# Kernel tuning notes

Measured on AMD Instinct MI355X. Metric: run time of the kernel, lower is better.

## Reference

```python
import jax, jax.numpy as jnp
import numpy as np

E = 1024   # n_embd
H = 16     # n_heads
D = 64     # head_dim
G = 4      # n_kv_groups
F = 4096   # ffn hidden_dim
V = 32000  # vocab
L = 4      # n_layers (all full_attention)
B = 1
T = 2048
ROT = 16   # partial_rotary_factor 0.25 * head_dim 64, rounded to even
EPS = 1e-6
THETA = 10000.0


def rope_tables(seq_len):
    # matches compute_rope_params: inv_freq over even indices of rotary_dim
    inv_freq = 1.0 / (THETA ** (jnp.arange(0, ROT, 2, dtype=jnp.float32) / ROT))
    ang = jnp.arange(seq_len, dtype=jnp.float32)[:, None] * inv_freq[None, :]
    ang = jnp.concatenate([ang, ang], axis=1)  # [T, ROT]
    return jnp.cos(ang), jnp.sin(ang)


def rmsnorm(x, w):
    # torch RMSNorm: x * rsqrt(mean(x^2)+eps) * (1 + weight)
    xf = x.astype(jnp.float32)
    n = xf * jax.lax.rsqrt(jnp.mean(xf * xf, axis=-1, keepdims=True) + EPS)
    return (n * (1.0 + w)).astype(x.dtype)


def apply_rope(x, cos, sin):
    # x: [B, h, T, D]; cos/sin: [1, 1, T, ROT]; partial rotary on first ROT dims
    x_rot, x_pass = x[..., :ROT], x[..., ROT:]
    x1, x2 = x_rot[..., :ROT // 2], x_rot[..., ROT // 2:]
    rotated = jnp.concatenate([-x2, x1], axis=-1)
    return jnp.concatenate([x_rot * cos + rotated * sin, x_pass], axis=-1)


def _forward(tokens, emb, Wq, Wk, Wv, Wo, qn, kn, n1, n2, f1, f2, f3, fn, head):
    cos, sin = rope_tables(T)
    cos = cos[None, None]  # [1,1,T,ROT]
    sin = sin[None, None]
    mask = jnp.triu(jnp.ones((T, T), dtype=bool), k=1)  # True = masked
    scale = D ** -0.5
    x = emb[tokens]  # [B,T,E]

    def block(x, p):
        wq, wk, wv, wo, qw, kw, w1, w2, g1, g2, g3 = p
        h = rmsnorm(x, w1)
        # fused Q + gate projection -> [B,T,H,2D], chunk on last dim
        qg = (h @ wq).reshape(B, T, H, 2 * D)
        q = qg[..., :D].transpose(0, 2, 1, 3)            # [B,H,T,D]
        gate = qg[..., D:].reshape(B, T, H * D)          # [B,T,H*D]
        k = (h @ wk).reshape(B, T, G, D).transpose(0, 2, 1, 3)  # [B,G,T,D]
        v = (h @ wv).reshape(B, T, G, D).transpose(0, 2, 1, 3)
        q = rmsnorm(q, qw)
        k = rmsnorm(k, kw)
        q = apply_rope(q, cos, sin)
        k = apply_rope(k, cos, sin)
        k = jnp.repeat(k, H // G, axis=1)  # GQA expand -> [B,H,T,D]
        v = jnp.repeat(v, H // G, axis=1)
        scores = jnp.einsum('bhqd,bhkd->bhqk', q, k)
        scores = jnp.where(mask, -jnp.inf, scores) * scale
        w = jax.nn.softmax(scores.astype(jnp.float32), axis=-1).astype(q.dtype)
        ctx = jnp.einsum('bhqk,bhkd->bhqd', w, v)
        ctx = ctx.transpose(0, 2, 1, 3).reshape(B, T, H * D)
        ctx = ctx * jax.nn.sigmoid(gate)
        x = x + ctx @ wo
        h2 = rmsnorm(x, w2)
        ff = (jax.nn.silu(h2 @ g1) * (h2 @ g2)) @ g3
        return x + ff, None

    params = (Wq, Wk, Wv, Wo, qn, kn, n1, n2, f1, f2, f3)
    x, _ = jax.lax.scan(block, x, params)
    return rmsnorm(x, fn) @ head  # logits [B,T,V]


def setup_inputs() -> dict:
    key = jax.random.key(0)
    ks = jax.random.split(key, 16)
    s = 0.02
    rn = lambda k, shape, sc=s: jax.random.normal(k, shape, jnp.float32) * sc
    return {
        'tokens': jax.random.randint(ks[0], (B, T), 0, V),
        'emb': rn(ks[1], (V, E)),
        'Wq': rn(ks[2], (L, E, 2 * H * D)),
        'Wk': rn(ks[3], (L, E, G * D)),
        'Wv': rn(ks[4], (L, E, G * D)),
        'Wo': rn(ks[5], (L, H * D, E)),
        'qn': rn(ks[6], (L, D)),
        'kn': rn(ks[7], (L, D)),
        'n1': rn(ks[8], (L, E)),
        'n2': rn(ks[9], (L, E)),
        'f1': rn(ks[10], (L, E, F)),
        'f2': rn(ks[11], (L, E, F)),
        'f3': rn(ks[12], (L, F, E)),
        'fn': rn(ks[13], (E,)),
        'head': rn(ks[14], (E, V)),
    }


def reference(tokens, emb, Wq, Wk, Wv, Wo, qn, kn, n1, n2, f1, f2, f3, fn, head):
    return _forward(tokens, emb, Wq, Wk, Wv, Wo, qn, kn, n1, n2, f1, f2, f3, fn, head)
```

## Files before the change

kernel.cpp:

```cpp
#include <hip/hip_runtime.h>

#define T_LEN 2048
#define E_DIM 1024
#define H_N 16
#define G_N 4
#define D_H 64
#define F_DIM 4096
#define V_SZ 32000
#define L_N 4

typedef __attribute__((ext_vector_type(8))) __bf16 bf16x8;
typedef __attribute__((ext_vector_type(4))) float f32x4;

__device__ __forceinline__ unsigned short f2bf(float f){
  unsigned int u = __float_as_uint(f);
  unsigned int r = (u + 0x7FFFu + ((u >> 16) & 1u)) >> 16;
  return (unsigned short)r;
}

__device__ __forceinline__ f32x4 mfma16(bf16x8 a, bf16x8 b, f32x4 c){
  return __builtin_amdgcn_mfma_f32_16x16x32_bf16(a, b, c, 0, 0, 0);
}

__device__ __forceinline__ void gl16(const void* g, void* l){
  __builtin_amdgcn_global_load_lds((const __attribute__((address_space(1))) void*)g,
                                   (__attribute__((address_space(3))) void*)l, 16, 0, 0);
}

#define SBAR() __builtin_amdgcn_s_barrier()
#define LGK0() do{ asm volatile("s_waitcnt lgkmcnt(0)" ::: "memory"); __builtin_amdgcn_sched_barrier(0); }while(0)
#define VMC4() do{ asm volatile("s_waitcnt vmcnt(4)" ::: "memory"); __builtin_amdgcn_sched_barrier(0); }while(0)
#define VMC0() do{ asm volatile("s_waitcnt vmcnt(0)" ::: "memory"); __builtin_amdgcn_sched_barrier(0); }while(0)

#define QSCALE 0.1803368801111183f

__global__ __launch_bounds__(256) void embed_k(const float* __restrict__ emb,
                                               const int* __restrict__ tokens,
                                               float* __restrict__ x){
  int t = blockIdx.x;
  int tok = tokens[t];
  const float4* src = (const float4*)(emb + (size_t)tok * E_DIM);
  float4* dst = (float4*)(x + (size_t)t * E_DIM);
  dst[threadIdx.x] = src[threadIdx.x];
}

__global__ __launch_bounds__(256) void transpose_bf16(const float* __restrict__ src,
                                                      unsigned short* __restrict__ dst,
                                                      int R, int C){
  __shared__ float tile[32][33];
  int c0 = blockIdx.x * 32, r0 = blockIdx.y * 32;
  int tx = threadIdx.x & 31, ty = threadIdx.x >> 5;
  for (int i = 0; i < 4; i++){
    int r = ty + i * 8;
    tile[r][tx] = src[(size_t)(r0 + r) * C + c0 + tx];
  }
  __syncthreads();
  for (int i = 0; i < 4; i++){
    int r = ty + i * 8;
    dst[(size_t)(c0 + r) * R + r0 + tx] = f2bf(tile[tx][r]);
  }
}

__device__ __forceinline__ void tr32(const float* __restrict__ src, unsigned short* __restrict__ dst,
                                     int R, int C, int bx, int by, float* tile ){
  int c0 = bx * 32, r0 = by * 32;
  int tx = threadIdx.x & 31, ty = threadIdx.x >> 5;
  for (int i = 0; i < 4; i++){
    int r = ty + i * 8;
    tile[r * 33 + tx] = src[(size_t)(r0 + r) * C + c0 + tx];
  }
  __syncthreads();
  for (int i = 0; i < 4; i++){
    int r = ty + i * 8;
    dst[(size_t)(c0 + r) * R + r0 + tx] = f2bf(tile[tx * 33 + r]);
  }
}

__global__ __launch_bounds__(256) void prep_weights(const float* __restrict__ Wq, const float* __restrict__ Wk,
                                                    const float* __restrict__ Wv, const float* __restrict__ Wo,
                                                    const float* __restrict__ f1, const float* __restrict__ f2,
                                                    const float* __restrict__ f3,
                                                    unsigned short* __restrict__ wt_qkv,
                                                    unsigned short* __restrict__ wt_o,
                                                    unsigned short* __restrict__ wt_f12i,
                                                    unsigned short* __restrict__ wt_f3){
  __shared__ float sh[1100];
  int id = blockIdx.x;
  if (id < 2048){ tr32(Wq, wt_qkv, 1024, 2048, id & 63, id >> 6, sh); return; }
  id -= 2048;
  if (id < 256){ tr32(Wk, wt_qkv + 2048 * 1024, 1024, 256, id & 7, id >> 3, sh); return; }
  id -= 256;
  if (id < 256){ tr32(Wv, wt_qkv + 2304 * 1024, 1024, 256, id & 7, id >> 3, sh); return; }
  id -= 256;
  if (id < 1024){ tr32(Wo, wt_o, 1024, 1024, id & 31, id >> 5, sh); return; }
  id -= 1024;
  if (id < 4096){ tr32(f3, wt_f3, 4096, 1024, id & 31, id >> 5, sh); return; }
  id -= 4096;
  {
    int q = id & 255, kb = id >> 8;
    float* t1 = sh; float* t2 = sh + 32 * 17;
    int c = threadIdx.x & 15, kk0 = threadIdx.x >> 4;
    for (int p = 0; p < 2; p++){
      int kk = p * 16 + kk0;
      t1[kk * 17 + c] = f1[(size_t)(kb * 32 + kk) * F_DIM + q * 16 + c];
      t2[kk * 17 + c] = f2[(size_t)(kb * 32 + kk) * F_DIM + q * 16 + c];
    }
    __syncthreads();
    int kk = threadIdx.x & 31, rb = threadIdx.x >> 5;
    for (int i = 0; i < 4; i++){
      int r = i * 8 + rb;
      float v = (r < 16) ? t1[kk * 17 + r] : t2[kk * 17 + (r - 16)];
      wt_f12i[(size_t)(q * 32 + r) * 1024 + kb * 32 + kk] = f2bf(v);
    }
  }
}

__global__ __launch_bounds__(256) void rmsnorm_k(const float* __restrict__ x,
                                                 const float* __restrict__ w,
                                                 unsigned short* __restrict__ out){
  const int t = blockIdx.x, tid = threadIdx.x;
  const float4 v = ((const float4*)(x + (size_t)t * E_DIM))[tid];
  float ss = v.x*v.x + v.y*v.y + v.z*v.z + v.w*v.w;
  for (int m = 1; m < 64; m <<= 1) ss += __shfl_xor(ss, m);
  __shared__ float red[4];
  if ((tid & 63) == 0) red[tid >> 6] = ss;
  __syncthreads();
  ss = red[0] + red[1] + red[2] + red[3];
  const float r = rsqrtf(ss * (1.0f / E_DIM) + 1e-6f);
  const float4 wv = ((const float4*)w)[tid];
  ushort4 o;
  o.x = f2bf(v.x * r * (1.0f + wv.x));
  o.y = f2bf(v.y * r * (1.0f + wv.y));
  o.z = f2bf(v.z * r * (1.0f + wv.z));
  o.w = f2bf(v.w * r * (1.0f + wv.w));
  ((ushort4*)(out + (size_t)t * E_DIM))[tid] = o;
}

template<bool ADD>
__global__ __launch_bounds__(256) void gemm64_bt(const unsigned short* __restrict__ A,
                                                 const unsigned short* __restrict__ Bt,
                                                 float* __restrict__ C,
                                                 int M, int N, int K){
  __shared__ unsigned short As[64 * 32];
  __shared__ unsigned short Bs[128 * 32];
  const int tid = threadIdx.x;
  const int lane = tid & 63, w = tid >> 6;
  const int l15 = lane & 15, l4 = lane >> 4;

  const int chunk = gridDim.x >> 3;
  const int wgid = (blockIdx.x & 7) * chunk + (blockIdx.x >> 3);
  const int nm = M >> 6;
  const int bm = wgid % nm, bn = wgid / nm;
  const int m0 = bm * 64, n0 = bn * 128;

  const int r0 = tid >> 2;
  const int c0 = (tid & 3) << 3;

  const unsigned short* gA  = A  + (size_t)(m0 + r0) * K + c0;
  const unsigned short* gB0 = Bt + (size_t)(n0 + r0) * K + c0;
  const unsigned short* gB1 = Bt + (size_t)(n0 + 64 + r0) * K + c0;
  unsigned short* lA  = As + w * 512;
  unsigned short* lB0 = Bs + w * 512;
  unsigned short* lB1 = Bs + 2048 + w * 512;

  f32x4 acc[4][2] = {};

  for (int k0 = 0; k0 < K; k0 += 32){
    __syncthreads();
    gl16(gA  + k0, lA);
    gl16(gB0 + k0, lB0);
    gl16(gB1 + k0, lB1);
    __syncthreads();
    bf16x8 af[4], bfr[2];
    for (int i = 0; i < 4; i++)
      af[i] = *(const bf16x8*)&As[(i * 16 + l15) * 32 + l4 * 8];
    for (int j = 0; j < 2; j++)
      bfr[j] = *(const bf16x8*)&Bs[(w * 32 + j * 16 + l15) * 32 + l4 * 8];
    for (int i = 0; i < 4; i++)
      for (int j = 0; j < 2; j++)
        acc[i][j] = mfma16(af[i], bfr[j], acc[i][j]);
  }

  for (int i = 0; i < 4; i++)
    for (int j = 0; j < 2; j++){
      int col = n0 + w * 32 + j * 16 + l15;
      for (int r = 0; r < 4; r++){
        int row = m0 + i * 16 + l4 * 4 + r;
        size_t idx = (size_t)row * N + col;
        if (ADD) C[idx] += acc[i][j][r]; else C[idx] = acc[i][j][r];
      }
    }
}

template<int EPI>
__global__ __launch_bounds__(512, 2) void gemm256(const unsigned short* __restrict__ A,
                                                  const unsigned short* __restrict__ Bt,
                                                  float* __restrict__ outF,
                                                  unsigned short* __restrict__ outH,
                                                  int M, int N, int K){
  __shared__ unsigned short lds[65536];
  const int tid = threadIdx.x;
  const int lane = tid & 63, w = tid >> 6;
  const int wm = w >> 2, wn = w & 3;
  const int l15 = lane & 15, l4 = lane >> 4;

  const int nwg = gridDim.x;
  const int xcd = (int)blockIdx.x & 7, lin = (int)blockIdx.x >> 3;
  const int q8 = nwg >> 3, r8 = nwg & 7;
  const int wgid = (xcd < r8 ? xcd * (q8 + 1) : r8 * (q8 + 1) + (xcd - r8) * q8) + lin;
  const int nm = M >> 8;
  const int bm = wgid % nm, bn = wgid / nm;
  const int m0 = bm * 256, n0 = bn * 256;
  const int NT = K >> 6;

  const int srow = (lane >> 3);
  const int scol = lane & 7;

  auto stageA = [&](int b, int h, int kt){
    #pragma unroll
    for (int c = 0; c < 2; c++){
      int r = w * 16 + c * 8 + srow;
      const unsigned short* g = A + (size_t)(m0 + h * 128 + r) * K + kt * 64 + ((scol ^ (r & 7)) << 3);
      gl16(g, (char*)lds + (b * 2 + h) * 16384 + (w * 16 + c * 8) * 128);
    }
  };
  auto stageB = [&](int b, int h, int kt){
    #pragma unroll
    for (int c = 0; c < 2; c++){
      int r = w * 16 + c * 8 + srow;
      const unsigned short* g = Bt + (size_t)(n0 + h * 128 + r) * K + kt * 64 + ((scol ^ (r & 7)) << 3);
      gl16(g, (char*)lds + 65536 + (b * 2 + h) * 16384 + (w * 16 + c * 8) * 128);
    }
  };

  const int sl0 = ((l4)     ^ (l15 & 7)) << 4;
  const int sl1 = ((4 | l4) ^ (l15 & 7)) << 4;

  f32x4 acc[8][4] = {};
  bf16x8 aF[8], bF[8];

  stageA(0, 0, 0); stageA(0, 1, 0); stageB(0, 0, 0); stageB(0, 1, 0);
  if (NT > 1){ stageB(1, 0, 1); stageB(1, 1, 1); }
  VMC4();
  SBAR();

  for (int kt = 0; kt < NT; kt++){
    const int buf = kt & 1;
    const char* Ab = (const char*)lds + (buf * 2 + wm) * 16384;
    const char* Bb = (const char*)lds + 65536 + (buf * 2 + (wn >> 1)) * 16384;
    const int brbase = (wn & 1) * 64;

    #pragma unroll
    for (int mf = 0; mf < 4; mf++){
      int r = mf * 16 + l15;
      aF[mf * 2 + 0] = *(const bf16x8*)(Ab + r * 128 + sl0);
      aF[mf * 2 + 1] = *(const bf16x8*)(Ab + r * 128 + sl1);
    }
    #pragma unroll
    for (int nf = 0; nf < 2; nf++){
      int r = brbase + nf * 16 + l15;
      bF[nf * 2 + 0] = *(const bf16x8*)(Bb + r * 128 + sl0);
      bF[nf * 2 + 1] = *(const bf16x8*)(Bb + r * 128 + sl1);
    }
    if (kt + 1 < NT) stageA(buf ^ 1, 0, kt + 1);
    SBAR(); LGK0();
    __builtin_amdgcn_s_setprio(1);
    #pragma unroll
    for (int mf = 0; mf < 4; mf++)
      #pragma unroll
      for (int nf = 0; nf < 2; nf++){
        acc[mf][nf] = mfma16(aF[mf * 2 + 0], bF[nf * 2 + 0], acc[mf][nf]);
        acc[mf][nf] = mfma16(aF[mf * 2 + 1], bF[nf * 2 + 1], acc[mf][nf]);
      }
    __builtin_amdgcn_s_setprio(0);
    SBAR();

    #pragma unroll
    for (int nf = 2; nf < 4; nf++){
      int r = brbase + nf * 16 + l15;
      bF[nf * 2 + 0] = *(const bf16x8*)(Bb + r * 128 + sl0);
      bF[nf * 2 + 1] = *(const bf16x8*)(Bb + r * 128 + sl1);
    }
    if (kt + 1 < NT) stageA(buf ^ 1, 1, kt + 1);
    SBAR(); LGK0();
    __builtin_amdgcn_s_setprio(1);
    #pragma unroll
    for (int mf = 0; mf < 4; mf++)
      #pragma unroll
      for (int nf = 2; nf < 4; nf++){
        acc[mf][nf] = mfma16(aF[mf * 2 + 0], bF[nf * 2 + 0], acc[mf][nf]);
        acc[mf][nf] = mfma16(aF[mf * 2 + 1], bF[nf * 2 + 1], acc[mf][nf]);
      }
    __builtin_amdgcn_s_setprio(0);
    SBAR();

    #pragma unroll
    for (int mf = 0; mf < 4; mf++){
      int r = 64 + mf * 16 + l15;
      aF[mf * 2 + 0] = *(const bf16x8*)(Ab + r * 128 + sl0);
      aF[mf * 2 + 1] = *(const bf16x8*)(Ab + r * 128 + sl1);
    }
    if (kt + 2 < NT) stageB(buf, 0, kt + 2);
    SBAR(); LGK0();
    __builtin_amdgcn_s_setprio(1);
    #pragma unroll
    for (int mf = 0; mf < 4; mf++)
      #pragma unroll
      for (int nf = 2; nf < 4; nf++){
        acc[4 + mf][nf] = mfma16(aF[mf * 2 + 0], bF[nf * 2 + 0], acc[4 + mf][nf]);
        acc[4 + mf][nf] = mfma16(aF[mf * 2 + 1], bF[nf * 2 + 1], acc[4 + mf][nf]);
      }
    __builtin_amdgcn_s_setprio(0);
    SBAR();

    if (kt + 2 < NT) stageB(buf, 1, kt + 2);
    SBAR();
    __builtin_amdgcn_s_setprio(1);
    #pragma unroll
    for (int mf = 0; mf < 4; mf++)
      #pragma unroll
      for (int nf = 0; nf < 2; nf++){
        acc[4 + mf][nf] = mfma16(aF[mf * 2 + 0], bF[nf * 2 + 0], acc[4 + mf][nf]);
        acc[4 + mf][nf] = mfma16(aF[mf * 2 + 1], bF[nf * 2 + 1], acc[4 + mf][nf]);
      }
    __builtin_amdgcn_s_setprio(0);
    if (kt + 2 < NT) { VMC4(); } else { VMC0(); }
    SBAR();
  }

  if (EPI == 0){
    #pragma unroll
    for (int mfg = 0; mfg < 8; mfg++){
      #pragma unroll
      for (int nf = 0; nf < 4; nf++){
        int col = n0 + wn * 64 + nf * 16 + l15;
        int row0 = m0 + wm * 128 + mfg * 16 + l4 * 4;
        #pragma unroll
        for (int r = 0; r < 4; r++)
          outF[(size_t)(row0 + r) * N + col] = acc[mfg][nf][r];
      }
    }
  } else {
    const int NH = N >> 1;
    #pragma unroll
    for (int mfg = 0; mfg < 8; mfg++){
      #pragma unroll
      for (int nfp = 0; nfp < 2; nfp++){
        int col = (n0 >> 1) + wn * 32 + nfp * 16 + l15;
        int row0 = m0 + wm * 128 + mfg * 16 + l4 * 4;
        #pragma unroll
        for (int r = 0; r < 4; r++){
          float u = acc[mfg][nfp * 2 + 0][r];
          float g = acc[mfg][nfp * 2 + 1][r];
          outH[(size_t)(row0 + r) * NH + col] = f2bf(u / (1.0f + __expf(-u)) * g);
        }
      }
    }
  }
}

__global__ __launch_bounds__(256) void qkvpost_k(const float* __restrict__ qkv,
                                                 const float* __restrict__ qn,
                                                 const float* __restrict__ kn,
                                                 unsigned short* __restrict__ qb,
                                                 unsigned short* __restrict__ kb,
                                                 unsigned short* __restrict__ vt){
  const int t = blockIdx.x;
  const int lane = threadIdx.x & 63, w = threadIdx.x >> 6;
  const int d = lane;
  const int fi = d & 7;
  const float invf = powf(10000.0f, -(float)fi * 0.125f);
  const float ang = (float)t * invf;
  const float c = cosf(ang), s = sinf(ang);

  for (int i = 0; i < 4; i++){
    int h = w * 4 + i;
    float v = qkv[(size_t)t * 2560 + h * 128 + d];
    float ss = v * v;
    for (int m = 1; m < 64; m <<= 1) ss += __shfl_xor(ss, m);
    float r = rsqrtf(ss * (1.0f / D_H) + 1e-6f);
    float xn = v * r * (1.0f + qn[d]);
    float partner = __shfl_xor(xn, 8);
    float o;
    if (d < 8)       o = xn * c - partner * s;
    else if (d < 16) o = xn * c + partner * s;
    else             o = xn;
    qb[((size_t)h * T_LEN + t) * D_H + d] = f2bf(o * QSCALE);
  }
  {
    float v = qkv[(size_t)t * 2560 + 2048 + w * 64 + d];
    float ss = v * v;
    for (int m = 1; m < 64; m <<= 1) ss += __shfl_xor(ss, m);
    float r = rsqrtf(ss * (1.0f / D_H) + 1e-6f);
    float xn = v * r * (1.0f + kn[d]);
    float partner = __shfl_xor(xn, 8);
    float o;
    if (d < 8)       o = xn * c - partner * s;
    else if (d < 16) o = xn * c + partner * s;
    else             o = xn;
    kb[((size_t)w * T_LEN + t) * D_H + d] = f2bf(o);
  }
  {
    float v = qkv[(size_t)t * 2560 + 2304 + w * 64 + d];
    vt[((size_t)(w * 64 + d)) * T_LEN + t] = f2bf(v);
  }
}

__global__ __launch_bounds__(256) void attn_k(const unsigned short* __restrict__ qb,
                                              const unsigned short* __restrict__ kb,
                                              const unsigned short* __restrict__ vt,
                                              const float* __restrict__ qkv,
                                              unsigned short* __restrict__ ctxg){
  const int qt = blockIdx.x, h = blockIdx.y;
  const int g = h >> 2;
  const int tid = threadIdx.x;
  const int wv = tid >> 6;
  const int lane = tid & 63;
  const int l15 = lane & 15, l4 = lane >> 4;
  const int q0 = qt * 16;
  const int nch = (q0 >> 6) + 1;

  __shared__ unsigned short Pl[4][16][72];
  __shared__ float sO[4][16][66];
  __shared__ float sM[4][16];
  __shared__ float sL[4][16];

  const bf16x8 aq0 = *(const bf16x8*)(qb + ((size_t)h * T_LEN + q0 + l15) * D_H + l4 * 8);
  const bf16x8 aq1 = *(const bf16x8*)(qb + ((size_t)h * T_LEN + q0 + l15) * D_H + 32 + l4 * 8);

  f32x4 acc[4] = {};
  float mrun[4], lpart[4];
  #pragma unroll
  for (int j = 0; j < 4; j++){ mrun[j] = -1e30f; lpart[j] = 0.0f; }

  for (int c = wv; c < nch; c += 4){
    const int kv0 = c << 6;
    f32x4 sc[4];
    #pragma unroll
    for (int cp = 0; cp < 4; cp++){
      const unsigned short* kbase = kb + ((size_t)g * T_LEN + kv0 + cp * 16 + l15) * D_H + l4 * 8;
      bf16x8 bk0 = *(const bf16x8*)(kbase);
      bf16x8 bk1 = *(const bf16x8*)(kbase + 32);
      f32x4 z = {0.f, 0.f, 0.f, 0.f};
      z = mfma16(aq0, bk0, z);
      z = mfma16(aq1, bk1, z);
      sc[cp] = z;
    }
    float resc[4];
    #pragma unroll
    for (int j = 0; j < 4; j++){
      int r = q0 + l4 * 4 + j;
      #pragma unroll
      for (int cp = 0; cp < 4; cp++){
        int col = kv0 + cp * 16 + l15;
        sc[cp][j] = (col <= r) ? sc[cp][j] : -1e30f;
      }
      float mx = fmaxf(fmaxf(sc[0][j], sc[1][j]), fmaxf(sc[2][j], sc[3][j]));
      for (int off = 1; off < 16; off <<= 1) mx = fmaxf(mx, __shfl_xor(mx, off));
      float mnew = fmaxf(mrun[j], mx);
      resc[j] = exp2f(mrun[j] - mnew);
      mrun[j] = mnew;
      float ssum = 0.0f;
      #pragma unroll
      for (int cp = 0; cp < 4; cp++){
        float pv = exp2f(sc[cp][j] - mnew);
        sc[cp][j] = pv;
        ssum += pv;
      }
      lpart[j] = lpart[j] * resc[j] + ssum;
      #pragma unroll
      for (int nt = 0; nt < 4; nt++) acc[nt][j] *= resc[j];
    }
    #pragma unroll
    for (int j = 0; j < 4; j++)
      #pragma unroll
      for (int cp = 0; cp < 4; cp++)
        Pl[wv][l4 * 4 + j][cp * 16 + l15] = f2bf(sc[cp][j]);
    asm volatile("s_waitcnt lgkmcnt(0)" ::: "memory");
    const bf16x8 pa0 = *(const bf16x8*)&Pl[wv][l15][l4 * 8];
    const bf16x8 pa1 = *(const bf16x8*)&Pl[wv][l15][32 + l4 * 8];
    #pragma unroll
    for (int nt = 0; nt < 4; nt++){
      const unsigned short* vbase = vt + ((size_t)g * 64 + nt * 16 + l15) * T_LEN + kv0;
      bf16x8 bv0 = *(const bf16x8*)(vbase + l4 * 8);
      bf16x8 bv1 = *(const bf16x8*)(vbase + 32 + l4 * 8);
      acc[nt] = mfma16(pa1, bv1, mfma16(pa0, bv0, acc[nt]));
    }
  }

  #pragma unroll
  for (int j = 0; j < 4; j++)
    for (int off = 1; off < 16; off <<= 1) lpart[j] += __shfl_xor(lpart[j], off);

  #pragma unroll
  for (int j = 0; j < 4; j++){
    int row = l4 * 4 + j;
    #pragma unroll
    for (int nt = 0; nt < 4; nt++)
      sO[wv][row][nt * 16 + l15] = acc[nt][j];
  }
  if (l15 == 0){
    #pragma unroll
    for (int j = 0; j < 4; j++){
      sM[wv][l4 * 4 + j] = mrun[j];
      sL[wv][l4 * 4 + j] = lpart[j];
    }
  }
  __syncthreads();

  #pragma unroll
  for (int rr = 0; rr < 4; rr++){
    int r = wv * 4 + rr;
    float m0 = sM[0][r], m1 = sM[1][r], m2 = sM[2][r], m3 = sM[3][r];
    float ms = fmaxf(fmaxf(m0, m1), fmaxf(m2, m3));
    float w0 = exp2f(m0 - ms), w1 = exp2f(m1 - ms), w2 = exp2f(m2 - ms), w3 = exp2f(m3 - ms);
    float accv = w0 * sO[0][r][lane] + w1 * sO[1][r][lane] + w2 * sO[2][r][lane] + w3 * sO[3][r][lane];
    float lsum = w0 * sL[0][r] + w1 * sL[1][r] + w2 * sL[2][r] + w3 * sL[3][r];
    float gate = qkv[(size_t)(q0 + r) * 2560 + h * 128 + 64 + lane];
    float val = accv / lsum * (1.0f / (1.0f + __expf(-gate)));
    ctxg[(size_t)(q0 + r) * (H_N * D_H) + h * D_H + lane] = f2bf(val);
  }
}

extern "C" void kernel_launch(void* const* d_in, const int* in_sizes, int n_in,
                              void* d_out, int out_size, void* d_ws, size_t ws_size,
                              hipStream_t stream){
  (void)in_sizes; (void)n_in; (void)out_size; (void)ws_size;
  const int*   tokens = (const int*)d_in[0];
  const float* emb    = (const float*)d_in[1];
  const float* Wq     = (const float*)d_in[2];
  const float* Wk     = (const float*)d_in[3];
  const float* Wv     = (const float*)d_in[4];
  const float* Wo     = (const float*)d_in[5];
  const float* qn     = (const float*)d_in[6];
  const float* kn     = (const float*)d_in[7];
  const float* n1     = (const float*)d_in[8];
  const float* n2     = (const float*)d_in[9];
  const float* f1     = (const float*)d_in[10];
  const float* f2     = (const float*)d_in[11];
  const float* f3     = (const float*)d_in[12];
  const float* fn     = (const float*)d_in[13];
  const float* head   = (const float*)d_in[14];
  float* out = (float*)d_out;

  char* ws = (char*)d_ws;
  size_t off = 0;
  auto alloc = [&](size_t bytes)->char*{
    char* p = ws + off;
    off += (bytes + 255) & ~(size_t)255;
    return p;
  };
  float*          x       = (float*)alloc((size_t)T_LEN * E_DIM * 4);
  unsigned short* hbf     = (unsigned short*)alloc((size_t)T_LEN * E_DIM * 2);
  float*          qkvf    = (float*)alloc((size_t)T_LEN * 2560 * 4);
  unsigned short* qb      = (unsigned short*)alloc((size_t)H_N * T_LEN * D_H * 2);
  unsigned short* kb      = (unsigned short*)alloc((size_t)G_N * T_LEN * D_H * 2);
  unsigned short* vt      = (unsigned short*)alloc((size_t)G_N * D_H * T_LEN * 2);
  unsigned short* ctxg    = (unsigned short*)alloc((size_t)T_LEN * E_DIM * 2);
  unsigned short* hg      = (unsigned short*)alloc((size_t)T_LEN * F_DIM * 2);
  unsigned short* wt_qkv  = (unsigned short*)alloc((size_t)2560 * E_DIM * 2);
  unsigned short* wt_o    = (unsigned short*)alloc((size_t)E_DIM * E_DIM * 2);
  unsigned short* wt_f12i = (unsigned short*)alloc((size_t)2 * F_DIM * E_DIM * 2);
  unsigned short* wt_f3   = (unsigned short*)alloc((size_t)E_DIM * F_DIM * 2);
  unsigned short* wt_head = (unsigned short*)alloc((size_t)V_SZ * E_DIM * 2);

  embed_k<<<T_LEN, 256, 0, stream>>>(emb, tokens, x);
  transpose_bf16<<<dim3(V_SZ / 32, E_DIM / 32), 256, 0, stream>>>(head, wt_head, E_DIM, V_SZ);

  for (int l = 0; l < L_N; l++){
    prep_weights<<<15872, 256, 0, stream>>>(Wq + (size_t)l * E_DIM * 2048,
                                            Wk + (size_t)l * E_DIM * 256,
                                            Wv + (size_t)l * E_DIM * 256,
                                            Wo + (size_t)l * E_DIM * E_DIM,
                                            f1 + (size_t)l * E_DIM * F_DIM,
                                            f2 + (size_t)l * E_DIM * F_DIM,
                                            f3 + (size_t)l * F_DIM * E_DIM,
                                            wt_qkv, wt_o, wt_f12i, wt_f3);

    rmsnorm_k<<<T_LEN, 256, 0, stream>>>(x, n1 + l * E_DIM, hbf);
    gemm64_bt<false><<<(T_LEN / 64) * (2560 / 128), 256, 0, stream>>>(hbf, wt_qkv, qkvf, T_LEN, 2560, E_DIM);
    qkvpost_k<<<T_LEN, 256, 0, stream>>>(qkvf, qn + l * D_H, kn + l * D_H, qb, kb, vt);
    attn_k<<<dim3(T_LEN / 16, H_N), 256, 0, stream>>>(qb, kb, vt, qkvf, ctxg);
    gemm64_bt<true><<<(T_LEN / 64) * (E_DIM / 128), 256, 0, stream>>>(ctxg, wt_o, x, T_LEN, E_DIM, E_DIM);

    rmsnorm_k<<<T_LEN, 256, 0, stream>>>(x, n2 + l * E_DIM, hbf);
    gemm256<1><<<(T_LEN / 256) * (2 * F_DIM / 256), 512, 0, stream>>>(hbf, wt_f12i, nullptr, hg, T_LEN, 2 * F_DIM, E_DIM);
    gemm64_bt<true><<<(T_LEN / 64) * (E_DIM / 128), 256, 0, stream>>>(hg, wt_f3, x, T_LEN, E_DIM, F_DIM);
  }

  rmsnorm_k<<<T_LEN, 256, 0, stream>>>(x, fn, hbf);
  gemm256<0><<<(T_LEN / 256) * (V_SZ / 256), 512, 0, stream>>>(hbf, wt_head, out, nullptr, T_LEN, V_SZ, E_DIM);
}
```

Before: 1.412 ms.

## Transpose QK^T MFMA so each lane owns one query row in attention softmax

```diff
diff --git a/kernel.cpp b/kernel.cpp
--- a/kernel.cpp
+++ b/kernel.cpp
@@ -16,6 +16,10 @@
   unsigned int u = __float_as_uint(f);
   unsigned int r = (u + 0x7FFFu + ((u >> 16) & 1u)) >> 16;
   return (unsigned short)r;
+}
+
+__device__ __forceinline__ unsigned int packbf(float a, float b){
+  return (unsigned int)f2bf(a) | ((unsigned int)f2bf(b) << 16);
 }
 
 __device__ __forceinline__ f32x4 mfma16(bf16x8 a, bf16x8 b, f32x4 c){
@@ -429,9 +433,7 @@
   const bf16x8 aq1 = *(const bf16x8*)(qb + ((size_t)h * T_LEN + q0 + l15) * D_H + 32 + l4 * 8);
 
   f32x4 acc[4] = {};
-  float mrun[4], lpart[4];
-  #pragma unroll
-  for (int j = 0; j < 4; j++){ mrun[j] = -1e30f; lpart[j] = 0.0f; }
+  float m = -1e30f, lpart = 0.0f;
 
   for (int c = wv; c < nch; c += 4){
     const int kv0 = c << 6;
@@ -442,40 +444,62 @@
       bf16x8 bk0 = *(const bf16x8*)(kbase);
       bf16x8 bk1 = *(const bf16x8*)(kbase + 32);
       f32x4 z = {0.f, 0.f, 0.f, 0.f};
-      z = mfma16(aq0, bk0, z);
-      z = mfma16(aq1, bk1, z);
+      z = mfma16(bk0, aq0, z);
+      z = mfma16(bk1, aq1, z);
       sc[cp] = z;
     }
-    float resc[4];
-    #pragma unroll
-    for (int j = 0; j < 4; j++){
-      int r = q0 + l4 * 4 + j;
-      #pragma unroll
-      for (int cp = 0; cp < 4; cp++){
-        int col = kv0 + cp * 16 + l15;
-        sc[cp][j] = (col <= r) ? sc[cp][j] : -1e30f;
-      }
-      float mx = fmaxf(fmaxf(sc[0][j], sc[1][j]), fmaxf(sc[2][j], sc[3][j]));
-      for (int off = 1; off < 16; off <<= 1) mx = fmaxf(mx, __shfl_xor(mx, off));
-      float mnew = fmaxf(mrun[j], mx);
-      resc[j] = exp2f(mrun[j] - mnew);
-      mrun[j] = mnew;
-      float ssum = 0.0f;
-      #pragma unroll
-      for (int cp = 0; cp < 4; cp++){
-        float pv = exp2f(sc[cp][j] - mnew);
-        sc[cp][j] = pv;
-        ssum += pv;
-      }
-      lpart[j] = lpart[j] * resc[j] + ssum;
-      #pragma unroll
-      for (int nt = 0; nt < 4; nt++) acc[nt][j] *= resc[j];
-    }
-    #pragma unroll
-    for (int j = 0; j < 4; j++)
+    if (c == nch - 1){
       #pragma unroll
       for (int cp = 0; cp < 4; cp++)
-        Pl[wv][l4 * 4 + j][cp * 16 + l15] = f2bf(sc[cp][j]);
+        #pragma unroll
+        for (int j = 0; j < 4; j++){
+          int kv = kv0 + cp * 16 + l4 * 4 + j;
+          sc[cp][j] = (kv <= q0 + l15) ? sc[cp][j] : -1e30f;
+        }
+    }
+    float mx = sc[0][0];
+    #pragma unroll
+    for (int cp = 0; cp < 4; cp++)
+      #pragma unroll
+      for (int j = 0; j < 4; j++) mx = fmaxf(mx, sc[cp][j]);
+    mx = fmaxf(mx, __shfl_xor(mx, 16));
+    mx = fmaxf(mx, __shfl_xor(mx, 32));
+    const float mnew = fmaxf(m, mx);
+    const bool grew = !__all(mnew == m);
+    const float mold = m;
+    m = mnew;
+
+    float ssum = 0.0f;
+    unsigned int up[4][2];
+    #pragma unroll
+    for (int cp = 0; cp < 4; cp++){
+      float p0 = exp2f(sc[cp][0] - mnew);
+      float p1 = exp2f(sc[cp][1] - mnew);
+      float p2 = exp2f(sc[cp][2] - mnew);
+      float p3 = exp2f(sc[cp][3] - mnew);
+      ssum += (p0 + p1) + (p2 + p3);
+      up[cp][0] = packbf(p0, p1);
+      up[cp][1] = packbf(p2, p3);
+    }
+    if (grew){
+      const float resc = exp2f(mold - mnew);
+      lpart *= resc;
+      float r0 = __shfl(resc, l4 * 4 + 0);
+      float r1 = __shfl(resc, l4 * 4 + 1);
+      float r2 = __shfl(resc, l4 * 4 + 2);
+      float r3 = __shfl(resc, l4 * 4 + 3);
+      #pragma unroll
+      for (int nt = 0; nt < 4; nt++){
+        acc[nt][0] *= r0; acc[nt][1] *= r1; acc[nt][2] *= r2; acc[nt][3] *= r3;
+      }
+    }
+    lpart += ssum;
+
+    #pragma unroll
+    for (int cp = 0; cp < 4; cp++){
+      uint2 pr; pr.x = up[cp][0]; pr.y = up[cp][1];
+      *(uint2*)&Pl[wv][l15][cp * 16 + l4 * 4] = pr;
+    }
     asm volatile("s_waitcnt lgkmcnt(0)" ::: "memory");
     const bf16x8 pa0 = *(const bf16x8*)&Pl[wv][l15][l4 * 8];
     const bf16x8 pa1 = *(const bf16x8*)&Pl[wv][l15][32 + l4 * 8];
@@ -488,9 +512,8 @@
     }
   }
 
-  #pragma unroll
-  for (int j = 0; j < 4; j++)
-    for (int off = 1; off < 16; off <<= 1) lpart[j] += __shfl_xor(lpart[j], off);
+  lpart += __shfl_xor(lpart, 16);
+  lpart += __shfl_xor(lpart, 32);
 
   #pragma unroll
   for (int j = 0; j < 4; j++){
@@ -499,12 +522,9 @@
     for (int nt = 0; nt < 4; nt++)
       sO[wv][row][nt * 16 + l15] = acc[nt][j];
   }
-  if (l15 == 0){
-    #pragma unroll
-    for (int j = 0; j < 4; j++){
-      sM[wv][l4 * 4 + j] = mrun[j];
-      sL[wv][l4 * 4 + j] = lpart[j];
-    }
+  if (l4 == 0){
+    sM[wv][l15] = m;
+    sL[wv][l15] = lpart;
   }
   __syncthreads();
 
```

Result: no change. 1.396 ms (-1.1%).
